# Kernel tuning notes

Measured on AMD Instinct MI355X. Metric: run time of the kernel, lower is better.

## Reference

```python
import jax, jax.numpy as jnp
import numpy as np

D = 768

def setup_inputs() -> dict:
    key = jax.random.key(0)
    ks = jax.random.split(key, 12)
    inp = {
        "text_embeddings": jax.random.normal(ks[0], (8, 512, D), dtype=jnp.float32),
        "kb_emb": jax.random.normal(ks[1], (200000, D), dtype=jnp.float32),
        "W_ret": jax.random.normal(ks[2], (D, D), dtype=jnp.float32) * 0.02,
        "b_ret": jax.random.normal(ks[3], (D,), dtype=jnp.float32) * 0.02,
        "Ws1": jax.random.normal(ks[4], (2 * D, D), dtype=jnp.float32) * 0.02,
        "bs1": jax.random.normal(ks[5], (D,), dtype=jnp.float32) * 0.02,
        "Ws2": jax.random.normal(ks[6], (D, 1), dtype=jnp.float32) * 0.02,
        "bs2": jax.random.normal(ks[7], (1,), dtype=jnp.float32) * 0.02,
        "mention_sent": jax.random.randint(ks[8], (256,), 0, 8, dtype=jnp.int32),
        "mention_start": jax.random.randint(ks[9], (256,), 0, 480, dtype=jnp.int32),
        "mention_len": jax.random.randint(ks[10], (256,), 0, 31, dtype=jnp.int32),
        "top_k": 100,
    }
    return inp


def reference(text_embeddings, kb_emb, W_ret, b_ret, Ws1, bs1, Ws2, bs2,
              mention_sent, mention_start, mention_len, top_k):
    S = text_embeddings.shape[1]
    pos = jnp.arange(S, dtype=jnp.int32)
    # inclusive span [start, start+len] -> mask [M, S]
    mask = (pos[None, :] >= mention_start[:, None]) & (pos[None, :] <= (mention_start + mention_len)[:, None])
    maskf = mask.astype(text_embeddings.dtype)
    sent = text_embeddings[mention_sent]                       # [M, S, D]
    mention_emb = jnp.einsum('msd,ms->md', sent, maskf) / maskf.sum(1, keepdims=True)

    # entity_retriever linear, then KB dot-product retrieval of top 2k candidates
    query = mention_emb @ W_ret.T + b_ret                      # [M, D]
    sims = query @ kb_emb.T                                    # [M, N]
    _, cand_idx = jax.lax.top_k(sims, 2 * top_k)               # [M, 2k]
    cand_embs = kb_emb[cand_idx]                               # [M, 2k, D]

    # candidate_scorer: Linear(2D->D) on concat(mention, cand) + ReLU + Linear(D->1) + Sigmoid
    m_part = mention_emb @ Ws1[:D]                             # [M, D]
    c_part = jnp.einsum('mkd,de->mke', cand_embs, Ws1[D:])     # [M, 2k, D]
    h = jax.nn.relu(m_part[:, None, :] + c_part + bs1)
    scores = jax.nn.sigmoid(jnp.einsum('mke,eo->mko', h, Ws2)[..., 0] + bs2[0])  # [M, 2k]

    top_scores, ti = jax.lax.top_k(scores, top_k)              # [M, k]
    top_kb_idx = jnp.take_along_axis(cand_idx, ti, axis=1)
    return top_scores, top_kb_idx
```

## Files before the change

kernel.cpp:

```cpp
#include <hip/hip_runtime.h>
#include <cfloat>
#include <cmath>
#include <cstdint>

#define DD 768
#define MM 256
#define NKB 200000
#define SLEN 512
#define KK 200
#define TOPK 100
#define SURV_CAP 1024
#define RESC 232
#define THRC 2.70f
#define MAXMARK 32768
#define DELTA 4e-5
#define NET 12

typedef __attribute__((ext_vector_type(8))) short bf16x8;
typedef __attribute__((ext_vector_type(4))) float f32x4;

__device__ __forceinline__ unsigned short f2bf_rne(float x) {
  unsigned u = __float_as_uint(x);
  unsigned r = (u + 0x7FFFu + ((u >> 16) & 1u)) >> 16;
  return (unsigned short)r;
}
__device__ __forceinline__ float bf2f(unsigned short us) {
  return __uint_as_float(((unsigned)us) << 16);
}
__device__ __forceinline__ void splitbf(float x, unsigned short& hi, unsigned short& lo) {
  hi = f2bf_rne(x);
  lo = f2bf_rne(x - bf2f(hi));
}

__global__ __launch_bounds__(256) void k_mention_emb(
    const float* __restrict__ text, const int* __restrict__ msent,
    const int* __restrict__ mstart, const int* __restrict__ mlen,
    double* __restrict__ me64) {
  int m = blockIdx.x;
  int sent = msent[m], st = mstart[m], ln = mlen[m];
  const float* base = text + (size_t)sent * SLEN * DD;
  for (int d = threadIdx.x; d < DD; d += blockDim.x) {
    double acc = 0.0;
    for (int s = st; s <= st + ln; ++s) acc += (double)base[(size_t)s * DD + d];
    me64[(size_t)m * DD + d] = acc / (double)(ln + 1);
  }
}

__global__ __launch_bounds__(256) void k_query(
    const double* __restrict__ me64, const float* __restrict__ Wret,
    const float* __restrict__ bret, double* __restrict__ q64,
    unsigned short* __restrict__ qb16, float* __restrict__ tthr) {
  int m = blockIdx.x;
  __shared__ double sme[DD];
  __shared__ float snorm[256];
  for (int d = threadIdx.x; d < DD; d += blockDim.x) sme[d] = me64[(size_t)m * DD + d];
  __syncthreads();
  float nloc = 0.f;
  for (int e = threadIdx.x; e < DD; e += blockDim.x) {
    double acc = (double)bret[e];
    const float* wr = Wret + (size_t)e * DD;
    for (int d = 0; d < DD; ++d) acc += sme[d] * (double)wr[d];
    q64[(size_t)m * DD + e] = acc;
    qb16[(size_t)m * DD + e] = f2bf_rne((float)acc);
    nloc += (float)(acc * acc);
  }
  snorm[threadIdx.x] = nloc; __syncthreads();
  for (int s = 128; s > 0; s >>= 1) {
    if (threadIdx.x < s) snorm[threadIdx.x] += snorm[threadIdx.x + s];
    __syncthreads();
  }
  if (threadIdx.x == 0) tthr[m] = THRC * sqrtf(snorm[0]);
}

__global__ __launch_bounds__(256) void k_mpart(
    const double* __restrict__ me64, const float* __restrict__ Ws1,
    double* __restrict__ mp64, float* __restrict__ mp32) {
  int m = blockIdx.x;
  __shared__ double sme[DD];
  for (int d = threadIdx.x; d < DD; d += blockDim.x) sme[d] = me64[(size_t)m * DD + d];
  __syncthreads();
  for (int e = threadIdx.x; e < DD; e += blockDim.x) {
    double acc = 0.0;
    for (int d = 0; d < DD; ++d) acc += sme[d] * (double)Ws1[(size_t)d * DD + e];
    mp64[(size_t)m * DD + e] = acc;
    mp32[(size_t)m * DD + e] = (float)acc;
  }
}

__global__ __launch_bounds__(256) void k_prep(
    const float* __restrict__ Ws1, unsigned short* __restrict__ Bth,
    unsigned short* __restrict__ Btl) {
  int e = blockIdx.x;
  for (int k = threadIdx.x; k < DD; k += 256) {
    float x = Ws1[(size_t)(DD + k) * DD + e];
    unsigned short hi, lo;
    splitbf(x, hi, lo);
    Bth[(size_t)e * DD + k] = hi;
    Btl[(size_t)e * DD + k] = lo;
  }
}

__global__ __launch_bounds__(512) void k_sims_mfma(
    const unsigned short* __restrict__ qb, const float* __restrict__ kb,
    const float* __restrict__ tthr, int* __restrict__ gcnt,
    uint2* __restrict__ gcand) {
  __shared__ unsigned short Bs[64 * 32];
  __shared__ float sthr[256];
  int n0 = blockIdx.x * 64;
  int tid = threadIdx.x;
  int lane = tid & 63, w = tid >> 6;
  int h = lane >> 4, c = lane & 15;
  if (tid < 256) sthr[tid] = tthr[tid];
  f32x4 acc[2][4] = {};
  const int brow = n0 + (tid >> 3);
  const int bk4  = (tid & 7) * 4;
  const int bwoff = ((tid >> 3) * 64 + (tid & 7) * 8) ^ (((tid >> 3) & 7) << 4);
  auto ldB = [&](int k0, float4 &dst) {
    dst = *(const float4*)(kb + (size_t)brow * DD + k0 + bk4);
  };
  auto stB = [&](const float4 &v) {
    uint2 p;
    p.x = (unsigned)f2bf_rne(v.x) | ((unsigned)f2bf_rne(v.y) << 16);
    p.y = (unsigned)f2bf_rne(v.z) | ((unsigned)f2bf_rne(v.w) << 16);
    *(uint2*)((char*)Bs + bwoff) = p;
  };
  const unsigned short* qa0 = qb + (size_t)(w * 32 + c) * DD;
  const unsigned short* qa1 = qb + (size_t)(w * 32 + 16 + c) * DD;
  auto step = [&](int k0, float4 &cur, float4 &nxt, bool pf) {
    bf16x8 a0 = *(const bf16x8*)(qa0 + k0 + h * 8);
    bf16x8 a1 = *(const bf16x8*)(qa1 + k0 + h * 8);
    __syncthreads();
    stB(cur);
    if (pf) ldB(k0 + 32, nxt);
    __syncthreads();
#pragma unroll
    for (int nf = 0; nf < 4; ++nf) {
      int n = nf * 16 + c;
      int off = (n * 64 + h * 16) ^ ((n & 7) << 4);
      bf16x8 b = *(bf16x8*)((char*)Bs + off);
      acc[0][nf] = __builtin_amdgcn_mfma_f32_16x16x32_bf16(a0, b, acc[0][nf], 0, 0, 0);
      acc[1][nf] = __builtin_amdgcn_mfma_f32_16x16x32_bf16(a1, b, acc[1][nf], 0, 0, 0);
    }
  };
  float4 b0, b1;
  ldB(0, b0);
#pragma unroll
  for (int kc = 0; kc < 12; ++kc) {
    step(kc * 64,      b0, b1, true);
    step(kc * 64 + 32, b1, b0, kc < 11);
  }
#pragma unroll
  for (int mf = 0; mf < 2; ++mf)
#pragma unroll
    for (int nf = 0; nf < 4; ++nf)
#pragma unroll
      for (int r = 0; r < 4; ++r) {
        int row = w * 32 + mf * 16 + h * 4 + r;
        int col = n0 + nf * 16 + c;
        float v = acc[mf][nf][r];
        if (v > sthr[row]) {
          int p = atomicAdd(&gcnt[row], 1);
          if (p < SURV_CAP) gcand[(size_t)row * SURV_CAP + p] = make_uint2(__float_as_uint(v), (unsigned)col);
        }
      }
}

__global__ __launch_bounds__(256) void k_select(
    const uint2* __restrict__ gcand, const int* __restrict__ gcnt,
    const float* __restrict__ kb, const double* __restrict__ q64,
    int* __restrict__ cidx) {
  int m = blockIdx.x;
  __shared__ float skf[SURV_CAP];
  __shared__ int   sidx[SURV_CAP];
  __shared__ double sq[DD];
  __shared__ double skey[256];
  __shared__ int    skidx[256];
  int tid = threadIdx.x;
  int cnt = gcnt[m]; if (cnt > SURV_CAP) cnt = SURV_CAP;
  for (int d = tid; d < DD; d += 256) sq[d] = q64[(size_t)m * DD + d];
  for (int i = tid; i < SURV_CAP; i += 256) {
    if (i < cnt) {
      uint2 v = gcand[(size_t)m * SURV_CAP + i];
      skf[i] = __uint_as_float(v.x);
      sidx[i] = (int)v.y;
    } else { skf[i] = -FLT_MAX; sidx[i] = 0x7fffffff; }
  }
  __syncthreads();
  for (int k = 2; k <= SURV_CAP; k <<= 1) {
    for (int j = k >> 1; j > 0; j >>= 1) {
      for (int i = tid; i < SURV_CAP; i += 256) {
        int l = i ^ j;
        if (l > i) {
          float ka = skf[i], kb2 = skf[l];
          int ia = sidx[i], ib = sidx[l];
          bool lBefore = (kb2 > ka) || (kb2 == ka && ib < ia);
          bool iBefore = (ka > kb2) || (ka == kb2 && ia < ib);
          bool dir = ((i & k) == 0);
          bool sw = dir ? lBefore : iBefore;
          if (sw) { skf[i] = kb2; skf[l] = ka; sidx[i] = ib; sidx[l] = ia; }
        }
      }
      __syncthreads();
    }
  }
  int lane = tid & 63, wv = tid >> 6;
  for (int cpos = wv; cpos < RESC; cpos += 4) {
    int ci = sidx[cpos];
    double s;
    if (ci < NKB) {
      const float* krow = kb + (size_t)ci * DD;
      double acc = 0.0;
      for (int d = lane; d < DD; d += 64) acc += sq[d] * (double)krow[d];
      for (int off2 = 32; off2 > 0; off2 >>= 1) acc += __shfl_down(acc, off2, 64);
      s = acc;
    } else s = -INFINITY;
    if (lane == 0) { skey[cpos] = s; skidx[cpos] = ci; }
  }
  if (tid >= RESC && tid < 256) { skey[tid] = -INFINITY; skidx[tid] = 0x7fffffff; }
  __syncthreads();
  for (int k = 2; k <= 256; k <<= 1) {
    for (int j = k >> 1; j > 0; j >>= 1) {
      int i = tid, l = i ^ j;
      if (l > i) {
        double ka = skey[i], kb2 = skey[l];
        int ia = skidx[i], ib = skidx[l];
        bool lBefore = (kb2 > ka) || (kb2 == ka && ib < ia);
        bool iBefore = (ka > kb2) || (ka == kb2 && ia < ib);
        bool dir = ((i & k) == 0);
        bool sw = dir ? lBefore : iBefore;
        if (sw) { skey[i] = kb2; skey[l] = ka; skidx[i] = ib; skidx[l] = ia; }
      }
      __syncthreads();
    }
  }
  for (int cc = tid; cc < KK; cc += 256) {
    int v = skidx[cc];
    cidx[(size_t)m * KK + cc] = (v < NKB) ? v : 0;
  }
}

__global__ __launch_bounds__(256) void k_score2(
    const float* __restrict__ kb, const int* __restrict__ cidx,
    const float* __restrict__ mp32, const unsigned short* __restrict__ Bth,
    const unsigned short* __restrict__ Btl, const float* __restrict__ bs1,
    const float* __restrict__ Ws2, float* __restrict__ gpart) {
  __shared__ unsigned short Ah[256 * 32], Al[256 * 32];
  __shared__ unsigned short Bh[64 * 32], Bl[64 * 32];
  __shared__ float smp[3][64], sb1v[64], sw2v[64];
  __shared__ int srow[256];
  int p = blockIdx.x;
  int x = p & 7, j = p >> 3;
  int ct = x + 8 * (j / NET), et = j % NET;
  int r0 = ct * 256, e0 = et * 64;
  int tid = threadIdx.x, lane = tid & 63, w = tid >> 6;
  int h = lane >> 4, c = lane & 15;
  srow[tid] = cidx[r0 + tid];
  int m0 = r0 / KK;
  int mm1 = (m0 + 1 < MM) ? m0 + 1 : MM - 1;
  int mm2 = (m0 + 2 < MM) ? m0 + 2 : MM - 1;
  if (tid < 64) {
    smp[0][tid] = mp32[(size_t)m0 * DD + e0 + tid];
    smp[1][tid] = mp32[(size_t)mm1 * DD + e0 + tid];
    smp[2][tid] = mp32[(size_t)mm2 * DD + e0 + tid];
    sb1v[tid] = bs1[e0 + tid];
    sw2v[tid] = Ws2[e0 + tid];
  }
  __syncthreads();
  const float* aaddr[8];
#pragma unroll
  for (int it = 0; it < 8; ++it) {
    int idx = tid + it * 256;
    int rr = idx >> 3, f4 = idx & 7;
    aaddr[it] = kb + (size_t)srow[rr] * DD + f4 * 4;
  }
  const int be = tid >> 2, bk8 = tid & 3;
  const unsigned short* bhaddr = Bth + (size_t)(e0 + be) * DD + bk8 * 8;
  const unsigned short* bladdr = Btl + (size_t)(e0 + be) * DD + bk8 * 8;
  float4 pa[8];
  uint4 pbh, pbl;
#pragma unroll
  for (int it = 0; it < 8; ++it) pa[it] = *(const float4*)(aaddr[it]);
  pbh = *(const uint4*)(bhaddr);
  pbl = *(const uint4*)(bladdr);
  f32x4 acc[4][4] = {};
  for (int k0 = 0; k0 < DD; k0 += 32) {
    __syncthreads();
#pragma unroll
    for (int it = 0; it < 8; ++it) {
      int idx = tid + it * 256;
      int rr = idx >> 3, f4 = idx & 7;
      float4 v = pa[it];
      unsigned short h0, h1, h2, h3, l0, l1, l2, l3;
      splitbf(v.x, h0, l0); splitbf(v.y, h1, l1);
      splitbf(v.z, h2, l2); splitbf(v.w, h3, l3);
      uint2 ph, pl;
      ph.x = (unsigned)h0 | ((unsigned)h1 << 16); ph.y = (unsigned)h2 | ((unsigned)h3 << 16);
      pl.x = (unsigned)l0 | ((unsigned)l1 << 16); pl.y = (unsigned)l2 | ((unsigned)l3 << 16);
      int off = (rr * 64 + f4 * 8) ^ ((rr & 7) << 4);
      *(uint2*)((char*)Ah + off) = ph;
      *(uint2*)((char*)Al + off) = pl;
    }
    {
      int off = (be * 64 + bk8 * 16) ^ ((be & 7) << 4);
      *(uint4*)((char*)Bh + off) = pbh;
      *(uint4*)((char*)Bl + off) = pbl;
    }
    if (k0 + 32 < DD) {
#pragma unroll
      for (int it = 0; it < 8; ++it) pa[it] = *(const float4*)(aaddr[it] + k0 + 32);
      pbh = *(const uint4*)(bhaddr + k0 + 32);
      pbl = *(const uint4*)(bladdr + k0 + 32);
    }
    __syncthreads();
    bf16x8 ah[4], al[4];
#pragma unroll
    for (int mf = 0; mf < 4; ++mf) {
      int rr = w * 64 + mf * 16 + c;
      int off = (rr * 64 + h * 16) ^ ((rr & 7) << 4);
      ah[mf] = *(bf16x8*)((char*)Ah + off);
      al[mf] = *(bf16x8*)((char*)Al + off);
    }
#pragma unroll
    for (int nf = 0; nf < 4; ++nf) {
      int e = nf * 16 + c;
      int off = (e * 64 + h * 16) ^ ((e & 7) << 4);
      bf16x8 bh = *(bf16x8*)((char*)Bh + off);
      bf16x8 bl = *(bf16x8*)((char*)Bl + off);
#pragma unroll
      for (int mf = 0; mf < 4; ++mf) {
        acc[mf][nf] = __builtin_amdgcn_mfma_f32_16x16x32_bf16(ah[mf], bh, acc[mf][nf], 0, 0, 0);
        acc[mf][nf] = __builtin_amdgcn_mfma_f32_16x16x32_bf16(ah[mf], bl, acc[mf][nf], 0, 0, 0);
        acc[mf][nf] = __builtin_amdgcn_mfma_f32_16x16x32_bf16(al[mf], bh, acc[mf][nf], 0, 0, 0);
      }
    }
  }
  int bnd1 = (m0 + 1) * KK, bnd2 = (m0 + 2) * KK;
#pragma unroll
  for (int mf = 0; mf < 4; ++mf) {
    float zp[4] = {0.f, 0.f, 0.f, 0.f};
#pragma unroll
    for (int nf = 0; nf < 4; ++nf) {
      int el = nf * 16 + c;
      float b1v = sb1v[el], w2v = sw2v[el];
#pragma unroll
      for (int r = 0; r < 4; ++r) {
        int rowg = r0 + w * 64 + mf * 16 + h * 4 + r;
        int sel = (rowg >= bnd1) + (rowg >= bnd2);
        float hh = acc[mf][nf][r] + smp[sel][el] + b1v;
        if (hh > 0.f) zp[r] += hh * w2v;
      }
    }
#pragma unroll
    for (int r = 0; r < 4; ++r) {
      float v = zp[r];
      v += __shfl_xor(v, 1, 64);
      v += __shfl_xor(v, 2, 64);
      v += __shfl_xor(v, 4, 64);
      v += __shfl_xor(v, 8, 64);
      if (c == 0)
        gpart[(size_t)(r0 + w * 64 + mf * 16 + h * 4 + r) * NET + et] = v;
    }
  }
}

__global__ __launch_bounds__(256) void k_zred(
    const float* __restrict__ gpart, const float* __restrict__ bs2,
    double* __restrict__ z64) {
  int r = blockIdx.x * 256 + threadIdx.x;
  double s = 0.0;
#pragma unroll
  for (int i = 0; i < NET; ++i) s += (double)gpart[(size_t)r * NET + i];
  z64[r] = s + (double)bs2[0];
}

__global__ __launch_bounds__(256) void k_mark(
    const double* __restrict__ z64, int* __restrict__ marks, int* __restrict__ mcnt) {
  int m = blockIdx.x;
  __shared__ double sk[256];
  __shared__ int sp[256];
  __shared__ int flag[256];
  int tid = threadIdx.x;
  flag[tid] = 0;
  if (tid < KK) { sk[tid] = z64[(size_t)m * KK + tid]; sp[tid] = tid; }
  else { sk[tid] = -INFINITY; sp[tid] = 0x7fffffff; }
  __syncthreads();
  for (int k = 2; k <= 256; k <<= 1) {
    for (int j = k >> 1; j > 0; j >>= 1) {
      int i = tid, l = i ^ j;
      if (l > i) {
        double ka = sk[i], kb2 = sk[l];
        int ia = sp[i], ib = sp[l];
        bool lBefore = (kb2 > ka) || (kb2 == ka && ib < ia);
        bool iBefore = (ka > kb2) || (ka == kb2 && ia < ib);
        bool dir = ((i & k) == 0);
        bool sw = dir ? lBefore : iBefore;
        if (sw) { sk[i] = kb2; sk[l] = ka; sp[i] = ib; sp[l] = ia; }
      }
      __syncthreads();
    }
  }
  if (tid <= 120) {
    if (sk[tid] - sk[tid + 1] < DELTA) {
      flag[tid] = 1;
      atomicExch(&flag[tid + 1], 1);
    }
  }
  __syncthreads();
  if (tid <= 121 && flag[tid]) {
    int p = atomicAdd(mcnt, 1);
    if (p < MAXMARK) marks[p] = m * KK + sp[tid];
  }
}

__global__ __launch_bounds__(256) void k_rescore(
    const float* __restrict__ kb, const int* __restrict__ cidx,
    const double* __restrict__ mp64, const float* __restrict__ Ws1,
    const float* __restrict__ bs1, const float* __restrict__ Ws2,
    const float* __restrict__ bs2, const int* __restrict__ marks,
    const int* __restrict__ mcnt, double* __restrict__ z64) {
  int cnt = *mcnt; if (cnt > MAXMARK) cnt = MAXMARK;
  __shared__ float sc[DD];
  __shared__ double sred[256];
  int tid = threadIdx.x;
  for (int it = blockIdx.x; it < cnt; it += gridDim.x) {
    int r = marks[it];
    int m = r / KK;
    int row = cidx[r];
    for (int d = tid; d < DD; d += 256) sc[d] = kb[(size_t)row * DD + d];
    __syncthreads();
    double pz = 0.0;
    for (int e = tid; e < DD; e += 256) {
      double a = 0.0;
      for (int d = 0; d < DD; ++d) a += (double)sc[d] * (double)Ws1[(size_t)(DD + d) * DD + e];
      double hv = mp64[(size_t)m * DD + e] + a + (double)bs1[e];
      if (hv > 0) pz += hv * (double)Ws2[e];
    }
    sred[tid] = pz; __syncthreads();
    for (int s = 128; s > 0; s >>= 1) { if (tid < s) sred[tid] += sred[tid + s]; __syncthreads(); }
    if (tid == 0) z64[r] = sred[0] + (double)bs2[0];
    __syncthreads();
  }
}

__global__ __launch_bounds__(256) void k_final(
    const double* __restrict__ z64, const int* __restrict__ cidx, float* __restrict__ out) {
  int m = blockIdx.x;
  __shared__ double sk[256];
  __shared__ int sp[256];
  int tid = threadIdx.x;
  if (tid < KK) { sk[tid] = z64[(size_t)m * KK + tid]; sp[tid] = tid; }
  else { sk[tid] = -INFINITY; sp[tid] = 0x7fffffff; }
  __syncthreads();
  for (int k = 2; k <= 256; k <<= 1) {
    for (int j = k >> 1; j > 0; j >>= 1) {
      int i = tid, l = i ^ j;
      if (l > i) {
        double ka = sk[i], kb2 = sk[l];
        int ia = sp[i], ib = sp[l];
        bool lBefore = (kb2 > ka) || (kb2 == ka && ib < ia);
        bool iBefore = (ka > kb2) || (ka == kb2 && ia < ib);
        bool dir = ((i & k) == 0);
        bool sw = dir ? lBefore : iBefore;
        if (sw) { sk[i] = kb2; sk[l] = ka; sp[i] = ib; sp[l] = ia; }
      }
      __syncthreads();
    }
  }
  if (tid < TOPK) {
    double z = sk[tid];
    out[(size_t)m * TOPK + tid] = (float)(1.0 / (1.0 + exp(-z)));
    out[(size_t)MM * TOPK + (size_t)m * TOPK + tid] = (float)cidx[(size_t)m * KK + sp[tid]];
  }
}

extern "C" void kernel_launch(void* const* d_in, const int* in_sizes, int n_in,
                              void* d_out, int out_size, void* d_ws, size_t ws_size,
                              hipStream_t stream) {
  const float* text  = (const float*)d_in[0];
  const float* kb    = (const float*)d_in[1];
  const float* Wret  = (const float*)d_in[2];
  const float* bret  = (const float*)d_in[3];
  const float* Ws1   = (const float*)d_in[4];
  const float* bs1   = (const float*)d_in[5];
  const float* Ws2   = (const float*)d_in[6];
  const float* bs2   = (const float*)d_in[7];
  const int* msent   = (const int*)d_in[8];
  const int* mstart  = (const int*)d_in[9];
  const int* mlen    = (const int*)d_in[10];
  float* out = (float*)d_out;

  char* ws = (char*)d_ws;
  size_t off = 0;
  auto alloc = [&](size_t bytes) -> void* {
    void* p = ws + off;
    off = (off + bytes + 255) & ~(size_t)255;
    return p;
  };
  double* me64 = (double*)alloc((size_t)MM * DD * 8);
  double* q64  = (double*)alloc((size_t)MM * DD * 8);
  unsigned short* qb16 = (unsigned short*)alloc((size_t)MM * DD * 2);
  float*  tthr = (float*) alloc((size_t)MM * 4);
  double* mp64 = (double*)alloc((size_t)MM * DD * 8);
  float*  mp32 = (float*) alloc((size_t)MM * DD * 4);
  int*    cidx = (int*)   alloc((size_t)MM * KK * 4);
  double* z64  = (double*)alloc((size_t)MM * KK * 8);
  float*  gpart = (float*)alloc((size_t)MM * KK * NET * 4);
  int*    marks = (int*)  alloc((size_t)MAXMARK * 4);
  int*    mcnt  = (int*)  alloc(256);
  int*    gcnt  = (int*)  alloc((size_t)MM * 4);
  uint2*  gcand = (uint2*)alloc((size_t)MM * SURV_CAP * 8);
  unsigned short* Bth = (unsigned short*)alloc((size_t)DD * DD * 2);
  unsigned short* Btl = (unsigned short*)alloc((size_t)DD * DD * 2);
  (void)ws_size;

  k_mention_emb<<<MM, 256, 0, stream>>>(text, msent, mstart, mlen, me64);
  k_query<<<MM, 256, 0, stream>>>(me64, Wret, bret, q64, qb16, tthr);
  k_mpart<<<MM, 256, 0, stream>>>(me64, Ws1, mp64, mp32);
  k_prep<<<DD, 256, 0, stream>>>(Ws1, Bth, Btl);

  hipMemsetAsync(gcnt, 0, (size_t)MM * 4, stream);
  k_sims_mfma<<<NKB / 64, 512, 0, stream>>>(qb16, kb, tthr, gcnt, gcand);
  k_select<<<MM, 256, 0, stream>>>(gcand, gcnt, kb, q64, cidx);

  k_score2<<<(MM * KK / 256) * NET, 256, 0, stream>>>(kb, cidx, mp32, Bth, Btl, bs1, Ws2, gpart);
  k_zred<<<MM * KK / 256, 256, 0, stream>>>(gpart, bs2, z64);
  hipMemsetAsync(mcnt, 0, 4, stream);
  k_mark<<<MM, 256, 0, stream>>>(z64, marks, mcnt);
  k_rescore<<<2048, 256, 0, stream>>>(kb, cidx, mp64, Ws1, bs1, Ws2, bs2, marks, mcnt, z64);
  k_final<<<MM, 256, 0, stream>>>(z64, cidx, out);
}
```

Measured before the change: 1.336 ms.

## Fuse front-end kernels and transpose W_ret for coalesced query projection

Merges the mention-embedding, query projection and mention-part projection into a single per-mention kernel that keeps the mean embedding in shared memory and computes both projections in one loop over d. W_ret is pre-transposed by a tiled transpose kernel so that reads across threads (indexed by e) are coalesced instead of strided by row. The z-reduction kernel is folded into the marking kernel. Together these remove launches and intermediate global round-trips and fix a badly strided W_ret access, at the cost of an extra transpose pass and more register pressure in the fused loop.

```diff
diff --git a/kernel.cpp b/kernel.cpp
--- a/kernel.cpp
+++ b/kernel.cpp
@@ -32,59 +32,62 @@
   lo = f2bf_rne(x - bf2f(hi));
 }
 
-__global__ __launch_bounds__(256) void k_mention_emb(
+__global__ __launch_bounds__(256) void k_prepT(
+    const float* __restrict__ Wret, float* __restrict__ WretT) {
+  __shared__ float tile[64][65];
+  int e0 = blockIdx.x * 64, d0 = blockIdx.y * 64;
+  int tid = threadIdx.x;
+  int r = tid >> 6, cc = tid & 63;
+  for (int i = 0; i < 64; i += 4)
+    tile[r + i][cc] = Wret[(size_t)(e0 + r + i) * DD + d0 + cc];
+  __syncthreads();
+  for (int i = 0; i < 64; i += 4)
+    WretT[(size_t)(d0 + r + i) * DD + e0 + cc] = tile[cc][r + i];
+}
+
+__global__ __launch_bounds__(256) void k_front(
     const float* __restrict__ text, const int* __restrict__ msent,
     const int* __restrict__ mstart, const int* __restrict__ mlen,
-    double* __restrict__ me64) {
-  int m = blockIdx.x;
-  int sent = msent[m], st = mstart[m], ln = mlen[m];
-  const float* base = text + (size_t)sent * SLEN * DD;
-  for (int d = threadIdx.x; d < DD; d += blockDim.x) {
-    double acc = 0.0;
-    for (int s = st; s <= st + ln; ++s) acc += (double)base[(size_t)s * DD + d];
-    me64[(size_t)m * DD + d] = acc / (double)(ln + 1);
-  }
-}
-
-__global__ __launch_bounds__(256) void k_query(
-    const double* __restrict__ me64, const float* __restrict__ Wret,
-    const float* __restrict__ bret, double* __restrict__ q64,
-    unsigned short* __restrict__ qb16, float* __restrict__ tthr) {
+    const float* __restrict__ WretT, const float* __restrict__ bret,
+    const float* __restrict__ Ws1,
+    double* __restrict__ q64, unsigned short* __restrict__ qb16,
+    float* __restrict__ tthr, double* __restrict__ mp64,
+    float* __restrict__ mp32) {
   int m = blockIdx.x;
   __shared__ double sme[DD];
   __shared__ float snorm[256];
-  for (int d = threadIdx.x; d < DD; d += blockDim.x) sme[d] = me64[(size_t)m * DD + d];
+  int tid = threadIdx.x;
+  {
+    int sent = msent[m], st = mstart[m], ln = mlen[m];
+    const float* base = text + (size_t)sent * SLEN * DD;
+    for (int d = tid; d < DD; d += 256) {
+      double acc = 0.0;
+      for (int s = st; s <= st + ln; ++s) acc += (double)base[(size_t)s * DD + d];
+      sme[d] = acc / (double)(ln + 1);
+    }
+  }
   __syncthreads();
   float nloc = 0.f;
-  for (int e = threadIdx.x; e < DD; e += blockDim.x) {
-    double acc = (double)bret[e];
-    const float* wr = Wret + (size_t)e * DD;
-    for (int d = 0; d < DD; ++d) acc += sme[d] * (double)wr[d];
-    q64[(size_t)m * DD + e] = acc;
-    qb16[(size_t)m * DD + e] = f2bf_rne((float)acc);
-    nloc += (float)(acc * acc);
-  }
-  snorm[threadIdx.x] = nloc; __syncthreads();
+  for (int e = tid; e < DD; e += 256) {
+    double aq = (double)bret[e];
+    double amp = 0.0;
+    for (int d = 0; d < DD; ++d) {
+      double md = sme[d];
+      aq  += md * (double)WretT[(size_t)d * DD + e];
+      amp += md * (double)Ws1[(size_t)d * DD + e];
+    }
+    q64[(size_t)m * DD + e] = aq;
+    qb16[(size_t)m * DD + e] = f2bf_rne((float)aq);
+    mp64[(size_t)m * DD + e] = amp;
+    mp32[(size_t)m * DD + e] = (float)amp;
+    nloc += (float)(aq * aq);
+  }
+  snorm[tid] = nloc; __syncthreads();
   for (int s = 128; s > 0; s >>= 1) {
-    if (threadIdx.x < s) snorm[threadIdx.x] += snorm[threadIdx.x + s];
-    __syncthreads();
-  }
-  if (threadIdx.x == 0) tthr[m] = THRC * sqrtf(snorm[0]);
-}
-
-__global__ __launch_bounds__(256) void k_mpart(
-    const double* __restrict__ me64, const float* __restrict__ Ws1,
-    double* __restrict__ mp64, float* __restrict__ mp32) {
-  int m = blockIdx.x;
-  __shared__ double sme[DD];
-  for (int d = threadIdx.x; d < DD; d += blockDim.x) sme[d] = me64[(size_t)m * DD + d];
-  __syncthreads();
-  for (int e = threadIdx.x; e < DD; e += blockDim.x) {
-    double acc = 0.0;
-    for (int d = 0; d < DD; ++d) acc += sme[d] * (double)Ws1[(size_t)d * DD + e];
-    mp64[(size_t)m * DD + e] = acc;
-    mp32[(size_t)m * DD + e] = (float)acc;
-  }
+    if (tid < s) snorm[tid] += snorm[tid + s];
+    __syncthreads();
+  }
+  if (tid == 0) tthr[m] = THRC * sqrtf(snorm[0]);
 }
 
 __global__ __launch_bounds__(256) void k_prep(
@@ -363,26 +366,23 @@
   }
 }
 
-__global__ __launch_bounds__(256) void k_zred(
+__global__ __launch_bounds__(256) void k_mark(
     const float* __restrict__ gpart, const float* __restrict__ bs2,
-    double* __restrict__ z64) {
-  int r = blockIdx.x * 256 + threadIdx.x;
-  double s = 0.0;
-#pragma unroll
-  for (int i = 0; i < NET; ++i) s += (double)gpart[(size_t)r * NET + i];
-  z64[r] = s + (double)bs2[0];
-}
-
-__global__ __launch_bounds__(256) void k_mark(
-    const double* __restrict__ z64, int* __restrict__ marks, int* __restrict__ mcnt) {
+    double* __restrict__ z64, int* __restrict__ marks, int* __restrict__ mcnt) {
   int m = blockIdx.x;
   __shared__ double sk[256];
   __shared__ int sp[256];
   __shared__ int flag[256];
   int tid = threadIdx.x;
   flag[tid] = 0;
-  if (tid < KK) { sk[tid] = z64[(size_t)m * KK + tid]; sp[tid] = tid; }
-  else { sk[tid] = -INFINITY; sp[tid] = 0x7fffffff; }
+  if (tid < KK) {
+    double s = 0.0;
+#pragma unroll
+    for (int i = 0; i < NET; ++i) s += (double)gpart[(size_t)(m * KK + tid) * NET + i];
+    s += (double)bs2[0];
+    z64[(size_t)m * KK + tid] = s;
+    sk[tid] = s; sp[tid] = tid;
+  } else { sk[tid] = -INFINITY; sp[tid] = 0x7fffffff; }
   __syncthreads();
   for (int k = 2; k <= 256; k <<= 1) {
     for (int j = k >> 1; j > 0; j >>= 1) {
@@ -496,7 +496,6 @@
     off = (off + bytes + 255) & ~(size_t)255;
     return p;
   };
-  double* me64 = (double*)alloc((size_t)MM * DD * 8);
   double* q64  = (double*)alloc((size_t)MM * DD * 8);
   unsigned short* qb16 = (unsigned short*)alloc((size_t)MM * DD * 2);
   float*  tthr = (float*) alloc((size_t)MM * 4);
@@ -511,21 +510,22 @@
   uint2*  gcand = (uint2*)alloc((size_t)MM * SURV_CAP * 8);
   unsigned short* Bth = (unsigned short*)alloc((size_t)DD * DD * 2);
   unsigned short* Btl = (unsigned short*)alloc((size_t)DD * DD * 2);
+  float*  WretT = (float*)alloc((size_t)DD * DD * 4);
   (void)ws_size;
 
-  k_mention_emb<<<MM, 256, 0, stream>>>(text, msent, mstart, mlen, me64);
-  k_query<<<MM, 256, 0, stream>>>(me64, Wret, bret, q64, qb16, tthr);
-  k_mpart<<<MM, 256, 0, stream>>>(me64, Ws1, mp64, mp32);
+  dim3 gt(DD / 64, DD / 64);
+  k_prepT<<<gt, 256, 0, stream>>>(Wret, WretT);
   k_prep<<<DD, 256, 0, stream>>>(Ws1, Bth, Btl);
+  k_front<<<MM, 256, 0, stream>>>(text, msent, mstart, mlen, WretT, bret, Ws1,
+                                  q64, qb16, tthr, mp64, mp32);
 
   hipMemsetAsync(gcnt, 0, (size_t)MM * 4, stream);
   k_sims_mfma<<<NKB / 64, 512, 0, stream>>>(qb16, kb, tthr, gcnt, gcand);
   k_select<<<MM, 256, 0, stream>>>(gcand, gcnt, kb, q64, cidx);
 
   k_score2<<<(MM * KK / 256) * NET, 256, 0, stream>>>(kb, cidx, mp32, Bth, Btl, bs1, Ws2, gpart);
-  k_zred<<<MM * KK / 256, 256, 0, stream>>>(gpart, bs2, z64);
   hipMemsetAsync(mcnt, 0, 4, stream);
-  k_mark<<<MM, 256, 0, stream>>>(z64, marks, mcnt);
+  k_mark<<<MM, 256, 0, stream>>>(gpart, bs2, z64, marks, mcnt);
   k_rescore<<<2048, 256, 0, stream>>>(kb, cidx, mp64, Ws1, bs1, Ws2, bs2, marks, mcnt, z64);
   k_final<<<MM, 256, 0, stream>>>(z64, cidx, out);
 }
```

Measured after the change: 1.305 ms. 1.02x faster.
